# Optimization experiments

Measured on AMD Instinct MI355X. Metric: run time of the kernel, lower is better.

## Reference

```python
import jax, jax.numpy as jnp
import numpy as np

ANCHORS = np.array([[[10, 13], [16, 30], [33, 23]],
                    [[30, 61], [62, 45], [59, 119]],
                    [[116, 90], [156, 198], [373, 326]]], dtype=np.float32)
STRIDES = [8, 16, 32]
NUM_CLASSES = 20
BOX_W, OBJ_W, CLS_W = 0.05, 1.5, 0.15
B, T = 16, 32


def setup_inputs() -> dict:
    key = jax.random.key(0)
    k0, k1, k2, kc, kxy, kwh = jax.random.split(key, 6)
    p0 = jax.random.normal(k0, (B, 75, 80, 80), dtype=jnp.float32)
    p1 = jax.random.normal(k1, (B, 75, 40, 40), dtype=jnp.float32)
    p2 = jax.random.normal(k2, (B, 75, 20, 20), dtype=jnp.float32)
    cls = jax.random.randint(kc, (B, T, 1), 0, NUM_CLASSES).astype(jnp.float32)
    txy = jax.random.uniform(kxy, (B, T, 2), dtype=jnp.float32)          # normalized centers
    twh = jax.random.uniform(kwh, (B, T, 2), dtype=jnp.float32) * 11.0 + 0.2  # grid-unit sizes
    targets = jnp.concatenate([cls, txy, twh], axis=-1)  # [B, T, 5]
    return {"p0": p0, "p1": p1, "p2": p2, "targets": targets}


def _bce_logits(x, t):
    # elementwise BCEWithLogits, numerically stable
    return jnp.maximum(x, 0.0) - x * t + jnp.log1p(jnp.exp(-jnp.abs(x)))


def _build_targets(targets, H, W, anchors_g, C):
    # targets: [B, T, 5] = (cls, tx, ty, tw, th); anchors_g: [3, 2] in grid units
    Bn, Tn = targets.shape[0], targets.shape[1]
    cls = targets[..., 0].astype(jnp.int32)
    tx, ty, tw, th = targets[..., 1], targets[..., 2], targets[..., 3], targets[..., 4]
    gx = jnp.clip(jnp.floor(tx * W).astype(jnp.int32), 0, W - 1)  # [B,T]
    gy = jnp.clip(jnp.floor(ty * H).astype(jnp.int32), 0, H - 1)
    aw, ah = anchors_g[:, 0], anchors_g[:, 1]                      # [3]
    inter = jnp.minimum(tw[..., None], aw) * jnp.minimum(th[..., None], ah)
    iou = inter / (tw[..., None] * th[..., None] + aw * ah - inter + 1e-6)  # [B,T,3]
    ba = jnp.argmax(iou, axis=-1)                                  # best anchor [B,T]
    valid = jnp.max(iou, axis=-1) > 0.3
    lin = (gy * W + gx) * 3 + ba                                   # [B,T]
    later = jnp.triu(jnp.ones((Tn, Tn), dtype=bool), 1)            # t' > t
    shadowed = jnp.any((lin[:, :, None] == lin[:, None, :]) & later & valid[:, None, :], axis=-1)
    valid = valid & ~shadowed
    baw = jnp.take(aw, ba)
    bah = jnp.take(ah, ba)
    tb = jnp.stack([tx * W - gx, ty * H - gy,
                    jnp.log(tw / baw + 1e-6), jnp.log(th / bah + 1e-6)], axis=-1)  # [B,T,4]
    b_idx = jnp.broadcast_to(jnp.arange(Bn)[:, None], (Bn, Tn))
    b_safe = jnp.where(valid, b_idx, Bn)  # out-of-bounds -> dropped
    tgt_boxes = jnp.zeros((Bn, H, W, 3, 4), jnp.float32).at[b_safe, gy, gx, ba].set(tb, mode='drop')
    tgt_obj = jnp.zeros((Bn, H, W, 3), jnp.float32).at[b_safe, gy, gx, ba].set(1.0, mode='drop')
    tgt_cls = jnp.zeros((Bn, H, W, 3, C), jnp.float32).at[b_safe, gy, gx, ba, cls].set(1.0, mode='drop')
    return tgt_boxes, tgt_obj, tgt_cls


def _yolo_loss(preds, targets):
    total = jnp.float32(0.0)
    for i, p in enumerate(preds):
        Bn, _, H, W = p.shape
        anchors_g = jnp.asarray(ANCHORS[i]) / STRIDES[i]
        pr = p.transpose(0, 2, 3, 1).reshape(Bn, H, W, 3, -1)  # [B,H,W,3,5+C]
        pred_boxes, pred_obj, pred_cls = pr[..., :4], pr[..., 4], pr[..., 5:]
        tgt_boxes, tgt_obj, tgt_cls = _build_targets(targets, H, W, anchors_g, NUM_CLASSES)
        obj_mask = (tgt_obj > 0.5).astype(jnp.float32)
        noobj_mask = 1.0 - obj_mask
        n_obj = obj_mask.sum() + 1e-6
        n_noobj = noobj_mask.sum() + 1e-6
        box_loss = jnp.sum((pred_boxes - tgt_boxes) ** 2) / n_obj  # unmasked sum, as in source
        bce_obj = _bce_logits(pred_obj, tgt_obj)
        obj_loss = jnp.sum(bce_obj * obj_mask) / n_obj
        noobj_loss = jnp.sum(bce_obj * noobj_mask) / n_noobj
        cls_loss = jnp.sum(_bce_logits(pred_cls, tgt_cls) * obj_mask[..., None]) / n_obj
        total = total + BOX_W * box_loss + OBJ_W * (obj_loss + 0.5 * noobj_loss) + CLS_W * cls_loss
    return total


def reference(p0, p1, p2, targets):
    return _yolo_loss([p0, p1, p2], targets)
```

## Files before the change

kernel.cpp:

```cpp
#include <hip/hip_runtime.h>

#define BN 16
#define TN 32
#define NCLS 20
#define NBLK 512
#define NTHR 256

__constant__ float c_aw[3][3] = {
  {1.25f,  2.0f,   4.125f},
  {1.875f, 3.875f, 3.6875f},
  {3.625f, 4.875f, 11.65625f}
};
__constant__ float c_ah[3][3] = {
  {1.625f,  3.75f,   2.875f},
  {3.8125f, 2.8125f, 7.4375f},
  {2.8125f, 6.1875f, 10.1875f}
};

__device__ __forceinline__ float bce(float x, float t){
  return fmaxf(x, 0.0f) - x * t + log1pf(__expf(-fabsf(x)));
}


__global__ __launch_bounds__(64)
void k_targets(const float* __restrict__ p0, const float* __restrict__ p1,
               const float* __restrict__ p2, const float* __restrict__ tg,
               float* __restrict__ ws){
  const int g      = blockIdx.x;
  const int tlevel = g >> 4;
  const int b      = g & 15;
  const int lane   = threadIdx.x;
  const int t      = (lane < 32) ? lane : 31;

  const float* p = (tlevel == 0) ? p0 : (tlevel == 1 ? p1 : p2);
  const int Hh   = (tlevel == 0) ? 80 : (tlevel == 1 ? 40 : 20);
  const int HW   = Hh * Hh;

  __shared__ int lin_s[32];

  const float cls_f = tg[(b*TN + t)*5 + 0];
  const float tx    = tg[(b*TN + t)*5 + 1];
  const float ty    = tg[(b*TN + t)*5 + 2];
  const float tw    = tg[(b*TN + t)*5 + 3];
  const float th    = tg[(b*TN + t)*5 + 4];

  int gx = (int)floorf(tx * (float)Hh); gx = min(max(gx, 0), Hh - 1);
  int gy = (int)floorf(ty * (float)Hh); gy = min(max(gy, 0), Hh - 1);

  float best = -1.0f; int ba = 0;
  #pragma unroll
  for (int a = 0; a < 3; ++a){
    float aw = c_aw[tlevel][a], ah = c_ah[tlevel][a];
    float inter = fminf(tw, aw) * fminf(th, ah);
    float iou = inter / (tw*th + aw*ah - inter + 1e-6f);
    if (iou > best){ best = iou; ba = a; }
  }
  const bool valid_pre = best > 0.3f;
  const int  lin = (gy * Hh + gx) * 3 + ba;

  if (lane < 32) lin_s[lane] = valid_pre ? lin : -1;
  __syncthreads();

  bool valid = (lane < 32) && valid_pre;
  if (valid){
    for (int u = t + 1; u < TN; ++u)
      if (lin_s[u] == lin){ valid = false; break; }
  }

  const size_t base = (size_t)(b*75 + ba*25) * HW + (size_t)(gy * Hh + gx);
  float xs[25];
  #pragma unroll
  for (int c = 0; c < 25; ++c) xs[c] = p[base + (size_t)c * HW];

  float v0 = 0.f, v1 = 0.f, v2 = 0.f, v3 = 0.f, v4 = 0.f;
  if (valid){
    const float baw = c_aw[tlevel][ba], bah = c_ah[tlevel][ba];
    float tb0 = tx * (float)Hh - (float)gx;
    float tb1 = ty * (float)Hh - (float)gy;
    float tb2 = logf(tw / baw + 1e-6f);
    float tb3 = logf(th / bah + 1e-6f);
    float d0 = xs[0]-tb0, d1 = xs[1]-tb1, d2 = xs[2]-tb2, d3 = xs[3]-tb3;
    v0 = (d0*d0 - xs[0]*xs[0]) + (d1*d1 - xs[1]*xs[1])
       + (d2*d2 - xs[2]*xs[2]) + (d3*d3 - xs[3]*xs[3]);
    v1 = bce(xs[4], 1.0f);
    v2 = bce(xs[4], 0.0f);
    const int cls = (int)cls_f;
    float cc = 0.f;
    #pragma unroll
    for (int c = 0; c < NCLS; ++c)
      cc += bce(xs[5 + c], (c == cls) ? 1.0f : 0.0f);
    v3 = cc;
    v4 = 1.0f;
  }

  #pragma unroll
  for (int off = 32; off > 0; off >>= 1){
    v0 += __shfl_down(v0, off, 64);
    v1 += __shfl_down(v1, off, 64);
    v2 += __shfl_down(v2, off, 64);
    v3 += __shfl_down(v3, off, 64);
    v4 += __shfl_down(v4, off, 64);
  }
  if (lane == 0){
    float* o = ws + 2048 + g*8;
    o[0] = v0; o[1] = v1; o[2] = v2; o[3] = v3; o[4] = v4;
  }
}

template<int HW4>
__device__ __forceinline__ void base_sum(const float* __restrict__ p, int lb, int nb,
                                         int tid, float& a0, float& a1){
  const int total = BN * 15 * HW4;
  for (int v = lb * NTHR + tid; v < total; v += nb * NTHR){
    const int run = v / (5 * HW4);
    const int off = v - run * (5 * HW4);
    const int c4  = off / HW4;
    const float4 x = ((const float4*)p)[(size_t)(25 * HW4) * run + off];
    if (c4 < 4) a0 += x.x*x.x + x.y*x.y + x.z*x.z + x.w*x.w;
    else        a1 += bce(x.x,0.f) + bce(x.y,0.f) + bce(x.z,0.f) + bce(x.w,0.f);
  }
}

__global__ __launch_bounds__(NTHR)
void k_base(const float* __restrict__ p0, const float* __restrict__ p1,
            const float* __restrict__ p2, float* __restrict__ ws){
  const int bid = blockIdx.x, tid = threadIdx.x;
  float a0 = 0.f, a1 = 0.f;
  if (bid < 390)      base_sum<1600>(p0, bid,       390, tid, a0, a1);
  else if (bid < 488) base_sum< 400>(p1, bid - 390,  98, tid, a0, a1);
  else                base_sum< 100>(p2, bid - 488,  24, tid, a0, a1);

  #pragma unroll
  for (int off = 32; off > 0; off >>= 1){
    a0 += __shfl_down(a0, off, 64);
    a1 += __shfl_down(a1, off, 64);
  }
  __shared__ float sm[8];
  const int wid = tid >> 6;
  if ((tid & 63) == 0){ sm[wid*2] = a0; sm[wid*2+1] = a1; }
  __syncthreads();
  if (tid == 0){
    ws[64 + bid*2 + 0] = sm[0] + sm[2] + sm[4] + sm[6];
    ws[64 + bid*2 + 1] = sm[1] + sm[3] + sm[5] + sm[7];
  }
}

__global__ __launch_bounds__(256)
void k_final(const float* __restrict__ ws, float* __restrict__ out){
  __shared__ float sb[6];
  __shared__ float st[24];
  const int tid = threadIdx.x;
  if (tid < 6)  sb[tid] = 0.f;
  if (tid < 24) st[tid] = 0.f;
  __syncthreads();

  for (int j = tid; j < NBLK; j += 256){
    const int lv = (j < 390) ? 0 : ((j < 488) ? 1 : 2);
    atomicAdd(&sb[lv*2 + 0], ws[64 + 2*j + 0]);
    atomicAdd(&sb[lv*2 + 1], ws[64 + 2*j + 1]);
  }
  if (tid < 48){
    const int tl = tid >> 4;
    #pragma unroll
    for (int m = 0; m < 5; ++m)
      atomicAdd(&st[tl*8 + m], ws[2048 + tid*8 + m]);
  }
  __syncthreads();

  if (tid == 0){
    const float cells[3] = {307200.f, 76800.f, 19200.f};
    float total = 0.f;
    for (int l = 0; l < 3; ++l){
      float Sbox  = sb[l*2 + 0] + st[l*8 + 0];
      float obj   = st[l*8 + 1];
      float noobj = sb[l*2 + 1] - st[l*8 + 2];
      float clsl  = st[l*8 + 3];
      float cnt   = st[l*8 + 4];
      float n_obj   = cnt + 1e-6f;
      float n_noobj = (cells[l] - cnt) + 1e-6f;
      total += 0.05f * Sbox / n_obj
             + 1.5f  * (obj / n_obj + 0.5f * noobj / n_noobj)
             + 0.15f * clsl / n_obj;
    }
    out[0] = total;
  }
}

extern "C" void kernel_launch(void* const* d_in, const int* in_sizes, int n_in,
                              void* d_out, int out_size, void* d_ws, size_t ws_size,
                              hipStream_t stream) {
  const float* p0 = (const float*)d_in[0];
  const float* p1 = (const float*)d_in[1];
  const float* p2 = (const float*)d_in[2];
  const float* tg = (const float*)d_in[3];
  float* out = (float*)d_out;
  float* ws  = (float*)d_ws;

  k_targets<<<48,   64,   0, stream>>>(p0, p1, p2, tg, ws);
  k_base   <<<NBLK, NTHR, 0, stream>>>(p0, p1, p2, ws);
  k_final  <<<1,    256,  0, stream>>>(ws, out);
}
```

Measured before the change: 96.93 us.

## Fuse target and base-sum kernels into one launch, use fast softplus

The separate target-gather kernel is merged into the base reduction kernel: the first 48 blocks handle per-target corrections and the remaining 512 do the streaming sums, removing one kernel launch and its serialization. The shadowing check now uses wave shuffles instead of shared memory plus a barrier. The streaming no-object BCE uses __logf(1+__expf) instead of log1pf, which is cheaper but slightly less accurate for large |x|. Target blocks launch with 256 threads and exit three waves early.

```diff
diff --git a/kernel.cpp b/kernel.cpp
--- a/kernel.cpp
+++ b/kernel.cpp
@@ -3,7 +3,7 @@
 #define BN 16
 #define TN 32
 #define NCLS 20
-#define NBLK 512
+#define NBASE 512
 #define NTHR 256
 
 __constant__ float c_aw[3][3] = {
@@ -21,91 +21,10 @@
   return fmaxf(x, 0.0f) - x * t + log1pf(__expf(-fabsf(x)));
 }
 
-
-__global__ __launch_bounds__(64)
-void k_targets(const float* __restrict__ p0, const float* __restrict__ p1,
-               const float* __restrict__ p2, const float* __restrict__ tg,
-               float* __restrict__ ws){
-  const int g      = blockIdx.x;
-  const int tlevel = g >> 4;
-  const int b      = g & 15;
-  const int lane   = threadIdx.x;
-  const int t      = (lane < 32) ? lane : 31;
-
-  const float* p = (tlevel == 0) ? p0 : (tlevel == 1 ? p1 : p2);
-  const int Hh   = (tlevel == 0) ? 80 : (tlevel == 1 ? 40 : 20);
-  const int HW   = Hh * Hh;
-
-  __shared__ int lin_s[32];
-
-  const float cls_f = tg[(b*TN + t)*5 + 0];
-  const float tx    = tg[(b*TN + t)*5 + 1];
-  const float ty    = tg[(b*TN + t)*5 + 2];
-  const float tw    = tg[(b*TN + t)*5 + 3];
-  const float th    = tg[(b*TN + t)*5 + 4];
-
-  int gx = (int)floorf(tx * (float)Hh); gx = min(max(gx, 0), Hh - 1);
-  int gy = (int)floorf(ty * (float)Hh); gy = min(max(gy, 0), Hh - 1);
-
-  float best = -1.0f; int ba = 0;
-  #pragma unroll
-  for (int a = 0; a < 3; ++a){
-    float aw = c_aw[tlevel][a], ah = c_ah[tlevel][a];
-    float inter = fminf(tw, aw) * fminf(th, ah);
-    float iou = inter / (tw*th + aw*ah - inter + 1e-6f);
-    if (iou > best){ best = iou; ba = a; }
-  }
-  const bool valid_pre = best > 0.3f;
-  const int  lin = (gy * Hh + gx) * 3 + ba;
-
-  if (lane < 32) lin_s[lane] = valid_pre ? lin : -1;
-  __syncthreads();
-
-  bool valid = (lane < 32) && valid_pre;
-  if (valid){
-    for (int u = t + 1; u < TN; ++u)
-      if (lin_s[u] == lin){ valid = false; break; }
-  }
-
-  const size_t base = (size_t)(b*75 + ba*25) * HW + (size_t)(gy * Hh + gx);
-  float xs[25];
-  #pragma unroll
-  for (int c = 0; c < 25; ++c) xs[c] = p[base + (size_t)c * HW];
-
-  float v0 = 0.f, v1 = 0.f, v2 = 0.f, v3 = 0.f, v4 = 0.f;
-  if (valid){
-    const float baw = c_aw[tlevel][ba], bah = c_ah[tlevel][ba];
-    float tb0 = tx * (float)Hh - (float)gx;
-    float tb1 = ty * (float)Hh - (float)gy;
-    float tb2 = logf(tw / baw + 1e-6f);
-    float tb3 = logf(th / bah + 1e-6f);
-    float d0 = xs[0]-tb0, d1 = xs[1]-tb1, d2 = xs[2]-tb2, d3 = xs[3]-tb3;
-    v0 = (d0*d0 - xs[0]*xs[0]) + (d1*d1 - xs[1]*xs[1])
-       + (d2*d2 - xs[2]*xs[2]) + (d3*d3 - xs[3]*xs[3]);
-    v1 = bce(xs[4], 1.0f);
-    v2 = bce(xs[4], 0.0f);
-    const int cls = (int)cls_f;
-    float cc = 0.f;
-    #pragma unroll
-    for (int c = 0; c < NCLS; ++c)
-      cc += bce(xs[5 + c], (c == cls) ? 1.0f : 0.0f);
-    v3 = cc;
-    v4 = 1.0f;
-  }
-
-  #pragma unroll
-  for (int off = 32; off > 0; off >>= 1){
-    v0 += __shfl_down(v0, off, 64);
-    v1 += __shfl_down(v1, off, 64);
-    v2 += __shfl_down(v2, off, 64);
-    v3 += __shfl_down(v3, off, 64);
-    v4 += __shfl_down(v4, off, 64);
-  }
-  if (lane == 0){
-    float* o = ws + 2048 + g*8;
-    o[0] = v0; o[1] = v1; o[2] = v2; o[3] = v3; o[4] = v4;
-  }
-}
+__device__ __forceinline__ float softplus_fast(float x){
+  return fmaxf(x, 0.0f) + __logf(1.0f + __expf(-fabsf(x)));
+}
+
 
 template<int HW4>
 __device__ __forceinline__ void base_sum(const float* __restrict__ p, int lb, int nb,
@@ -117,18 +36,104 @@
     const int c4  = off / HW4;
     const float4 x = ((const float4*)p)[(size_t)(25 * HW4) * run + off];
     if (c4 < 4) a0 += x.x*x.x + x.y*x.y + x.z*x.z + x.w*x.w;
-    else        a1 += bce(x.x,0.f) + bce(x.y,0.f) + bce(x.z,0.f) + bce(x.w,0.f);
+    else        a1 += softplus_fast(x.x) + softplus_fast(x.y)
+                    + softplus_fast(x.z) + softplus_fast(x.w);
   }
 }
 
 __global__ __launch_bounds__(NTHR)
-void k_base(const float* __restrict__ p0, const float* __restrict__ p1,
-            const float* __restrict__ p2, float* __restrict__ ws){
-  const int bid = blockIdx.x, tid = threadIdx.x;
+void k_main(const float* __restrict__ p0, const float* __restrict__ p1,
+            const float* __restrict__ p2, const float* __restrict__ tg,
+            float* __restrict__ ws){
+  const int bid = blockIdx.x;
+  const int tid = threadIdx.x;
+
+  if (bid < 48){
+    if (tid >= 64) return;
+    const int g      = bid;
+    const int tlevel = g >> 4;
+    const int b      = g & 15;
+    const int lane   = tid;
+    const int t      = (lane < 32) ? lane : 31;
+
+    const float* p = (tlevel == 0) ? p0 : (tlevel == 1 ? p1 : p2);
+    const int Hh   = (tlevel == 0) ? 80 : (tlevel == 1 ? 40 : 20);
+    const int HW   = Hh * Hh;
+
+    const float cls_f = tg[(b*TN + t)*5 + 0];
+    const float tx    = tg[(b*TN + t)*5 + 1];
+    const float ty    = tg[(b*TN + t)*5 + 2];
+    const float tw    = tg[(b*TN + t)*5 + 3];
+    const float th    = tg[(b*TN + t)*5 + 4];
+
+    int gx = (int)floorf(tx * (float)Hh); gx = min(max(gx, 0), Hh - 1);
+    int gy = (int)floorf(ty * (float)Hh); gy = min(max(gy, 0), Hh - 1);
+
+    float best = -1.0f; int ba = 0;
+    #pragma unroll
+    for (int a = 0; a < 3; ++a){
+      float aw = c_aw[tlevel][a], ah = c_ah[tlevel][a];
+      float inter = fminf(tw, aw) * fminf(th, ah);
+      float iou = inter / (tw*th + aw*ah - inter + 1e-6f);
+      if (iou > best){ best = iou; ba = a; }
+    }
+    const bool valid_pre = best > 0.3f;
+    const int  lin = (gy * Hh + gx) * 3 + ba;
+
+    int lin_v = (valid_pre && lane < 32) ? lin : -1;
+    bool valid = valid_pre && (lane < 32);
+    #pragma unroll 1
+    for (int u = 1; u < TN; ++u){
+      int other = __shfl(lin_v, u, 64);
+      if (valid && u > t && other == lin) valid = false;
+    }
+
+    const size_t base = (size_t)(b*75 + ba*25) * HW + (size_t)(gy * Hh + gx);
+    float xs[25];
+    #pragma unroll
+    for (int c = 0; c < 25; ++c) xs[c] = p[base + (size_t)c * HW];
+
+    float v0 = 0.f, v1 = 0.f, v2 = 0.f, v3 = 0.f, v4 = 0.f;
+    if (valid){
+      const float baw = c_aw[tlevel][ba], bah = c_ah[tlevel][ba];
+      float tb0 = tx * (float)Hh - (float)gx;
+      float tb1 = ty * (float)Hh - (float)gy;
+      float tb2 = logf(tw / baw + 1e-6f);
+      float tb3 = logf(th / bah + 1e-6f);
+      float d0 = xs[0]-tb0, d1 = xs[1]-tb1, d2 = xs[2]-tb2, d3 = xs[3]-tb3;
+      v0 = (d0*d0 - xs[0]*xs[0]) + (d1*d1 - xs[1]*xs[1])
+         + (d2*d2 - xs[2]*xs[2]) + (d3*d3 - xs[3]*xs[3]);
+      v1 = bce(xs[4], 1.0f);
+      v2 = bce(xs[4], 0.0f);
+      const int cls = (int)cls_f;
+      float cc = 0.f;
+      #pragma unroll
+      for (int c = 0; c < NCLS; ++c)
+        cc += bce(xs[5 + c], (c == cls) ? 1.0f : 0.0f);
+      v3 = cc;
+      v4 = 1.0f;
+    }
+
+    #pragma unroll
+    for (int off = 32; off > 0; off >>= 1){
+      v0 += __shfl_down(v0, off, 64);
+      v1 += __shfl_down(v1, off, 64);
+      v2 += __shfl_down(v2, off, 64);
+      v3 += __shfl_down(v3, off, 64);
+      v4 += __shfl_down(v4, off, 64);
+    }
+    if (lane == 0){
+      float* o = ws + 2048 + g*8;
+      o[0] = v0; o[1] = v1; o[2] = v2; o[3] = v3; o[4] = v4;
+    }
+    return;
+  }
+
+  const int j = bid - 48;
   float a0 = 0.f, a1 = 0.f;
-  if (bid < 390)      base_sum<1600>(p0, bid,       390, tid, a0, a1);
-  else if (bid < 488) base_sum< 400>(p1, bid - 390,  98, tid, a0, a1);
-  else                base_sum< 100>(p2, bid - 488,  24, tid, a0, a1);
+  if (j < 390)      base_sum<1600>(p0, j,       390, tid, a0, a1);
+  else if (j < 488) base_sum< 400>(p1, j - 390,  98, tid, a0, a1);
+  else              base_sum< 100>(p2, j - 488,  24, tid, a0, a1);
 
   #pragma unroll
   for (int off = 32; off > 0; off >>= 1){
@@ -140,8 +145,8 @@
   if ((tid & 63) == 0){ sm[wid*2] = a0; sm[wid*2+1] = a1; }
   __syncthreads();
   if (tid == 0){
-    ws[64 + bid*2 + 0] = sm[0] + sm[2] + sm[4] + sm[6];
-    ws[64 + bid*2 + 1] = sm[1] + sm[3] + sm[5] + sm[7];
+    ws[64 + j*2 + 0] = sm[0] + sm[2] + sm[4] + sm[6];
+    ws[64 + j*2 + 1] = sm[1] + sm[3] + sm[5] + sm[7];
   }
 }
 
@@ -154,7 +159,7 @@
   if (tid < 24) st[tid] = 0.f;
   __syncthreads();
 
-  for (int j = tid; j < NBLK; j += 256){
+  for (int j = tid; j < NBASE; j += 256){
     const int lv = (j < 390) ? 0 : ((j < 488) ? 1 : 2);
     atomicAdd(&sb[lv*2 + 0], ws[64 + 2*j + 0]);
     atomicAdd(&sb[lv*2 + 1], ws[64 + 2*j + 1]);
@@ -196,7 +201,6 @@
   float* out = (float*)d_out;
   float* ws  = (float*)d_ws;
 
-  k_targets<<<48,   64,   0, stream>>>(p0, p1, p2, tg, ws);
-  k_base   <<<NBLK, NTHR, 0, stream>>>(p0, p1, p2, ws);
-  k_final  <<<1,    256,  0, stream>>>(ws, out);
-}
+  k_main <<<48 + NBASE, NTHR, 0, stream>>>(p0, p1, p2, tg, ws);
+  k_final<<<1,          256,  0, stream>>>(ws, out);
+}
```

Result: faster. 90.09 us (-7.1%).
